# Performance work log

Hardware: AMD Instinct MI355X
Metric: run time of the kernel (lower is better)

The kernel has to match this reference:

```python
import jax, jax.numpy as jnp
import numpy as np

TRIM = 0.2
EPS = 1e-06
BIG = 1e30  # sentinel pushing invalid pixels to the end of the sort


def setup_inputs() -> dict:
    key = jax.random.key(0)
    k1, k2, k3 = jax.random.split(key, 3)
    B, C, H, W = 32, 1, 384, 1280
    pred = jax.random.normal(k1, (B, C, H, W), dtype=jnp.float32)
    gt = jax.random.normal(k2, (B, C, H, W), dtype=jnp.float32)
    mask = jax.random.randint(k3, (B, C, H, W), 0, 2, dtype=jnp.int32)
    return {"pred": pred, "gt": gt, "mask": mask}


def _per_sample_loss(p, g, m):
    # p, g: [N] float; m: [N] bool
    mf = m.astype(p.dtype)
    n = mf.sum()                      # number of valid pixels (float)
    n_safe = jnp.maximum(n, 1.0)
    # masked least-squares scale/shift: alpha = cov(d,z)/var(d), beta = mean_z - alpha*mean_d
    mean_d = jnp.sum(p * mf) / n_safe
    mean_z = jnp.sum(g * mf) / n_safe
    var_d = jnp.sum(p * p * mf) / n_safe - mean_d * mean_d
    cov_dz = jnp.sum(p * g * mf) / n_safe - mean_d * mean_z
    alpha = cov_dz / (var_d + EPS)
    beta = mean_z - alpha * mean_d
    # residuals; invalid pixels pushed to the tail of the sort
    res = jnp.abs(alpha * p + beta - g)
    res = jnp.where(m, res, BIG)
    res_sorted = jnp.sort(res)
    # keep the k = floor((1-trim)*n) smallest residuals
    k = jnp.floor((1.0 - TRIM) * n).astype(jnp.int32)
    keep = jnp.arange(res.shape[0], dtype=jnp.int32) < k
    kept_sum = jnp.sum(jnp.where(keep, res_sorted, 0.0))
    mean_kept = kept_sum / jnp.maximum(k.astype(p.dtype), 1.0)
    return jnp.where(k > 0, mean_kept, 0.0)


def reference(pred, gt, mask):
    B = pred.shape[0]
    p = pred.reshape(B, -1)
    g = gt.reshape(B, -1)
    m = mask.reshape(B, -1) > 0
    per_b = jax.vmap(_per_sample_loss)(p, g, m)  # [B]
    return jnp.mean(per_b)
```

## Files before the change

### kernel.cpp

```cpp
#include <hip/hip_runtime.h>
#include <stdint.h>

#define NB 32
#define NPIX 491520
#define NT 256

#define K1CHUNKS 60
#define K1CHUNK 8192
#define K1HALF4 (K1CHUNK / 8)
#define K1GROUPS (K1CHUNK / 4)
#define K1WORDS (K1CHUNK / 64)

#define K2CHUNKS 32
#define K2CHUNK 15360
#define K2IT (K2CHUNK / 4 / NT)
#define K2WORDS (K2CHUNK / 64)

#define NBINS 4096

#define CNT1 (1ull << 40)
#define SLOWMASK ((1ull << 40) - 1ull)

typedef float  vf4 __attribute__((ext_vector_type(4)));
typedef int    vi4 __attribute__((ext_vector_type(4)));

struct Ws {
  double moments[NB][5];
  double losses[NB];
  unsigned long long hist64[NB][NBINS];
};

__device__ __forceinline__ double wave_sum_d(double v) {
#pragma unroll
  for (int o = 32; o > 0; o >>= 1) v += __shfl_down(v, o, 64);
  return v;
}

__device__ __forceinline__ double block_sum_d(double v, double* red4) {
  v = wave_sum_d(v);
  const int lane = threadIdx.x & 63, w = threadIdx.x >> 6;
  if (lane == 0) red4[w] = v;
  __syncthreads();
  return red4[0] + red4[1] + red4[2] + red4[3];
}

__device__ __forceinline__ int k_from_n(double n) {
  return (int)floorf(0.8f * (float)n);
}

__device__ __forceinline__ void coef_from_moments(const Ws* ws, int b, float* a_out, float* be_out) {
  const double n = ws->moments[b][0];
  const double ns = n > 1.0 ? n : 1.0;
  const double md = ws->moments[b][1] / ns;
  const double mz = ws->moments[b][2] / ns;
  const double var = ws->moments[b][3] / ns - md * md;
  const double cov = ws->moments[b][4] / ns - md * mz;
  const double a = cov / (var + 1e-6);
  *a_out = (float)a;
  *be_out = (float)(mz - a * md);
}

__device__ __forceinline__ double bin_sum(int bin, unsigned long long h) {
  const double cnt = (double)(h >> 40);
  const double slow = (double)(h & SLOWMASK);
  const int e = bin >> 4, t4 = bin & 15;
  if (e == 0)
    return ldexp(cnt * (double)(t4 << 19) + slow, -149);
  return ldexp(cnt * (1.0 + (double)t4 * 0.0625) + slow * (1.0 / 8388608.0), e - 127);
}

template <bool BM>
__global__ __launch_bounds__(NT, 8) void k_mom(
    const float* __restrict__ pred, const float* __restrict__ gt,
    const int* __restrict__ mask, Ws* __restrict__ ws,
    unsigned long long* __restrict__ bm) {
  const int b = blockIdx.y;
  const size_t base = (size_t)b * NPIX + (size_t)blockIdx.x * K1CHUNK;
  const vf4* p4 = (const vf4*)(pred + base);
  const vf4* g4 = (const vf4*)(gt + base);
  const vi4* m4 = (const vi4*)(mask + base);
  __shared__ unsigned char nib[K1GROUPS];
  __shared__ double red4[4];
  float n = 0.f, sp = 0.f, sg = 0.f, spp = 0.f, spg = 0.f;
  for (int i = threadIdx.x; i < K1HALF4; i += NT) {
    vf4 pa = __builtin_nontemporal_load(&p4[i]);
    vf4 pb = __builtin_nontemporal_load(&p4[i + K1HALF4]);
    vf4 ga = __builtin_nontemporal_load(&g4[i]);
    vf4 gb = __builtin_nontemporal_load(&g4[i + K1HALF4]);
    vi4 ma = __builtin_nontemporal_load(&m4[i]);
    vi4 mb = __builtin_nontemporal_load(&m4[i + K1HALF4]);
    const float pe[8] = {pa.x, pa.y, pa.z, pa.w, pb.x, pb.y, pb.z, pb.w};
    const float ge[8] = {ga.x, ga.y, ga.z, ga.w, gb.x, gb.y, gb.z, gb.w};
    const int   me[8] = {ma.x, ma.y, ma.z, ma.w, mb.x, mb.y, mb.z, mb.w};
#pragma unroll
    for (int j = 0; j < 8; j++) {
      const float mf = me[j] ? 1.f : 0.f;
      const float pm = pe[j] * mf;
      const float gm = ge[j] * mf;
      n += mf; sp += pm; sg += gm;
      spp = fmaf(pe[j], pm, spp);
      spg = fmaf(pe[j], gm, spg);
    }
    if (BM) {
      nib[i] = (unsigned char)((me[0] ? 1 : 0) | (me[1] ? 2 : 0) |
                               (me[2] ? 4 : 0) | (me[3] ? 8 : 0));
      nib[i + K1HALF4] = (unsigned char)((me[4] ? 1 : 0) | (me[5] ? 2 : 0) |
                                         (me[6] ? 4 : 0) | (me[7] ? 8 : 0));
    }
  }
  if (BM) {
    __syncthreads();
    if (threadIdx.x < K1WORDS) {
      unsigned long long w = 0;
#pragma unroll
      for (int j = 0; j < 16; j++)
        w |= (unsigned long long)nib[threadIdx.x * 16 + j] << (4 * j);
      bm[base / 64 + threadIdx.x] = w;
    }
    __syncthreads();
  }
  double v[5] = {(double)n, (double)sp, (double)sg, (double)spp, (double)spg};
#pragma unroll
  for (int q = 0; q < 5; q++) {
    const double s = block_sum_d(v[q], red4);
    if (threadIdx.x == 0) atomicAdd(&ws->moments[b][q], s);
    __syncthreads();
  }
  const int flat = (b * K1CHUNKS + (int)blockIdx.x) * NT + (int)threadIdx.x;
  if (flat < NB * NBINS) ((unsigned long long*)ws->hist64)[flat] = 0ull;
}

template <bool BM>
__global__ __launch_bounds__(NT, 4) void k_hist(
    const float* __restrict__ pred, const float* __restrict__ gt,
    const int* __restrict__ mask, const unsigned long long* __restrict__ bm,
    Ws* __restrict__ ws) {
  __shared__ unsigned long long h64[NBINS];
  __shared__ unsigned long long smask[K2WORDS];
  for (int i = threadIdx.x; i < NBINS; i += NT) h64[i] = 0ull;
  const int b = blockIdx.y;
  const size_t base = (size_t)b * NPIX + (size_t)blockIdx.x * K2CHUNK;
  if (BM) {
    if (threadIdx.x < K2WORDS) smask[threadIdx.x] = bm[base / 64 + threadIdx.x];
  }
  float a, be;
  coef_from_moments(ws, b, &a, &be);
  __syncthreads();
  const vf4* p4 = (const vf4*)(pred + base);
  const vf4* g4 = (const vf4*)(gt + base);
  const vi4* m4 = (const vi4*)(mask + base);
  for (int j = 0; j < K2IT; j++) {
    const int i = j * NT + (int)threadIdx.x;
    const vf4 p = __builtin_nontemporal_load(&p4[i]);
    const vf4 g = __builtin_nontemporal_load(&g4[i]);
    const float pe[4] = {p.x, p.y, p.z, p.w};
    const float ge[4] = {g.x, g.y, g.z, g.w};
    int me[4];
    if (BM) {
      const unsigned int nb4 =
          (unsigned int)(smask[i >> 4] >> ((i & 15) * 4)) & 0xFu;
      me[0] = nb4 & 1; me[1] = nb4 & 2; me[2] = nb4 & 4; me[3] = nb4 & 8;
    } else {
      const vi4 m = __builtin_nontemporal_load(&m4[i]);
      me[0] = m.x; me[1] = m.y; me[2] = m.z; me[3] = m.w;
    }
#pragma unroll
    for (int l = 0; l < 4; l++) {
      if (!me[l]) continue;
      const float r = fabsf(fmaf(a, pe[l], be) - ge[l]);
      const uint32_t t = __float_as_uint(r);
      atomicAdd(&h64[t >> 19], CNT1 | (unsigned long long)(t & 0x7FFFFu));
    }
  }
  __syncthreads();
  for (int i = threadIdx.x; i < NBINS; i += NT) {
    const unsigned long long v = h64[i];
    if (v) atomicAdd(&ws->hist64[b][i], v);
  }
}

__global__ __launch_bounds__(NT) void k_fin(Ws* __restrict__ ws) {
  const int b = (int)blockIdx.x;
  const int tid = (int)threadIdx.x;
  __shared__ int pc[NT];
  __shared__ int shX, shCum;
  __shared__ double red4[4];
  const unsigned long long* H = ws->hist64[b];
  unsigned long long h[16];
  int lc = 0;
#pragma unroll
  for (int j = 0; j < 16; j++) { h[j] = H[tid * 16 + j]; lc += (int)(h[j] >> 40); }
  pc[tid] = lc;
  if (tid == 0) { shX = NBINS; shCum = 0; }
  __syncthreads();
  int pre = 0;
  for (int t = 0; t < tid; t++) pre += pc[t];
  const int k = k_from_n(ws->moments[b][0]);
  if (k > 0 && pre < k && pre + lc >= k) {
    int cum = pre;
#pragma unroll
    for (int j = 0; j < 16; j++) {
      const int c = (int)(h[j] >> 40);
      if (cum + c >= k) { shX = tid * 16 + j; shCum = cum; break; }
      cum += c;
    }
  }
  __syncthreads();
  const int X = shX;
  double below = 0.0;
#pragma unroll
  for (int j = 0; j < 16; j++) {
    const int idx = tid * 16 + j;
    if (idx < X) below += bin_sum(idx, h[j]);
  }
  const double tot = block_sum_d(below, red4);
  if (tid == 0) {
    double loss = 0.0;
    if (k > 0 && X < NBINS) {
      const unsigned long long hX = H[X];
      const double cX = (double)(hX >> 40);
      const double partial = (double)(k - shCum) * (bin_sum(X, hX) / cX);
      loss = (tot + partial) / (double)k;
    }
    ws->losses[b] = loss;
  }
}

__global__ void k_out(const Ws* __restrict__ ws, float* __restrict__ out) {
  double v = (threadIdx.x < NB) ? ws->losses[threadIdx.x] : 0.0;
  v = wave_sum_d(v);
  if (threadIdx.x == 0) out[0] = (float)(v / (double)NB);
}

extern "C" void kernel_launch(void* const* d_in, const int* in_sizes, int n_in,
                              void* d_out, int out_size, void* d_ws, size_t ws_size,
                              hipStream_t stream) {
  const float* pred = (const float*)d_in[0];
  const float* gt   = (const float*)d_in[1];
  const int*   mask = (const int*)d_in[2];
  float* out = (float*)d_out;
  Ws* ws = (Ws*)d_ws;

  const size_t boff = (sizeof(Ws) + 255) & ~(size_t)255;
  const size_t bbytes = (size_t)NB * NPIX / 8;
  const bool bm_ok = ws_size >= boff + bbytes;
  unsigned long long* bm = (unsigned long long*)((char*)d_ws + boff);

  (void)hipMemsetAsync(d_ws, 0, sizeof(double) * NB * 6, stream);

  dim3 g1(K1CHUNKS, NB);
  dim3 g2(K2CHUNKS, NB);
  if (bm_ok) {
    k_mom<true><<<g1, NT, 0, stream>>>(pred, gt, mask, ws, bm);
    k_hist<true><<<g2, NT, 0, stream>>>(pred, gt, mask, bm, ws);
  } else {
    k_mom<false><<<g1, NT, 0, stream>>>(pred, gt, mask, ws, nullptr);
    k_hist<false><<<g2, NT, 0, stream>>>(pred, gt, mask, nullptr, ws);
  }
  k_fin<<<NB, NT, 0, stream>>>(ws);
  k_out<<<1, 64, 0, stream>>>(ws, out);
}
```

Measured before the change: 209.6 us.

## Halve chunk sizes, use cached loads in moments pass, fold final reduction into k_fin

Grid chunk sizes for the moments and histogram kernels are halved, doubling the block count for better occupancy and load balance. The moments kernel unrolls its loop and drops nontemporal hints on pred/gt so the second pass can hit those lines in cache. The separate output kernel is removed: k_fin atomically accumulates per-sample losses and the last block writes the mean, saving one launch. Finer chunks double the atomics on moments and histograms, and the last-block pattern adds a fence and a counter that the memset must clear.

```diff
diff --git a/kernel.cpp b/kernel.cpp
--- a/kernel.cpp
+++ b/kernel.cpp
@@ -5,14 +5,14 @@
 #define NPIX 491520
 #define NT 256
 
-#define K1CHUNKS 60
-#define K1CHUNK 8192
+#define K1CHUNKS 120
+#define K1CHUNK 4096
 #define K1HALF4 (K1CHUNK / 8)
 #define K1GROUPS (K1CHUNK / 4)
 #define K1WORDS (K1CHUNK / 64)
 
-#define K2CHUNKS 32
-#define K2CHUNK 15360
+#define K2CHUNKS 60
+#define K2CHUNK 8192
 #define K2IT (K2CHUNK / 4 / NT)
 #define K2WORDS (K2CHUNK / 64)
 
@@ -26,7 +26,8 @@
 
 struct Ws {
   double moments[NB][5];
-  double losses[NB];
+  double loss_sum;
+  unsigned long long done;
   unsigned long long hist64[NB][NBINS];
 };
 
@@ -82,11 +83,14 @@
   __shared__ unsigned char nib[K1GROUPS];
   __shared__ double red4[4];
   float n = 0.f, sp = 0.f, sg = 0.f, spp = 0.f, spg = 0.f;
-  for (int i = threadIdx.x; i < K1HALF4; i += NT) {
-    vf4 pa = __builtin_nontemporal_load(&p4[i]);
-    vf4 pb = __builtin_nontemporal_load(&p4[i + K1HALF4]);
-    vf4 ga = __builtin_nontemporal_load(&g4[i]);
-    vf4 gb = __builtin_nontemporal_load(&g4[i + K1HALF4]);
+  const int t = (int)threadIdx.x;
+#pragma unroll
+  for (int u = 0; u < 2; u++) {
+    const int i = t + u * NT;
+    vf4 pa = p4[i];
+    vf4 pb = p4[i + K1HALF4];
+    vf4 ga = g4[i];
+    vf4 gb = g4[i + K1HALF4];
     vi4 ma = __builtin_nontemporal_load(&m4[i]);
     vi4 mb = __builtin_nontemporal_load(&m4[i + K1HALF4]);
     const float pe[8] = {pa.x, pa.y, pa.z, pa.w, pb.x, pb.y, pb.z, pb.w};
@@ -110,12 +114,12 @@
   }
   if (BM) {
     __syncthreads();
-    if (threadIdx.x < K1WORDS) {
+    if (t < K1WORDS) {
       unsigned long long w = 0;
 #pragma unroll
       for (int j = 0; j < 16; j++)
-        w |= (unsigned long long)nib[threadIdx.x * 16 + j] << (4 * j);
-      bm[base / 64 + threadIdx.x] = w;
+        w |= (unsigned long long)nib[t * 16 + j] << (4 * j);
+      bm[base / 64 + t] = w;
     }
     __syncthreads();
   }
@@ -123,10 +127,10 @@
 #pragma unroll
   for (int q = 0; q < 5; q++) {
     const double s = block_sum_d(v[q], red4);
-    if (threadIdx.x == 0) atomicAdd(&ws->moments[b][q], s);
+    if (t == 0) atomicAdd(&ws->moments[b][q], s);
     __syncthreads();
   }
-  const int flat = (b * K1CHUNKS + (int)blockIdx.x) * NT + (int)threadIdx.x;
+  const int flat = (b * K1CHUNKS + (int)blockIdx.x) * NT + t;
   if (flat < NB * NBINS) ((unsigned long long*)ws->hist64)[flat] = 0ull;
 }
 
@@ -149,6 +153,7 @@
   const vf4* p4 = (const vf4*)(pred + base);
   const vf4* g4 = (const vf4*)(gt + base);
   const vi4* m4 = (const vi4*)(mask + base);
+#pragma unroll 2
   for (int j = 0; j < K2IT; j++) {
     const int i = j * NT + (int)threadIdx.x;
     const vf4 p = __builtin_nontemporal_load(&p4[i]);
@@ -179,7 +184,7 @@
   }
 }
 
-__global__ __launch_bounds__(NT) void k_fin(Ws* __restrict__ ws) {
+__global__ __launch_bounds__(NT) void k_fin(Ws* __restrict__ ws, float* __restrict__ out) {
   const int b = (int)blockIdx.x;
   const int tid = (int)threadIdx.x;
   __shared__ int pc[NT];
@@ -222,14 +227,15 @@
       const double partial = (double)(k - shCum) * (bin_sum(X, hX) / cX);
       loss = (tot + partial) / (double)k;
     }
-    ws->losses[b] = loss;
-  }
-}
-
-__global__ void k_out(const Ws* __restrict__ ws, float* __restrict__ out) {
-  double v = (threadIdx.x < NB) ? ws->losses[threadIdx.x] : 0.0;
-  v = wave_sum_d(v);
-  if (threadIdx.x == 0) out[0] = (float)(v / (double)NB);
+    atomicAdd(&ws->loss_sum, loss);
+    __threadfence();
+    const unsigned long long old = atomicAdd(&ws->done, 1ull);
+    if (old == (unsigned long long)(NB - 1)) {
+      __threadfence();
+      const double sum = atomicAdd(&ws->loss_sum, 0.0);
+      out[0] = (float)(sum / (double)NB);
+    }
+  }
 }
 
 extern "C" void kernel_launch(void* const* d_in, const int* in_sizes, int n_in,
@@ -246,7 +252,7 @@
   const bool bm_ok = ws_size >= boff + bbytes;
   unsigned long long* bm = (unsigned long long*)((char*)d_ws + boff);
 
-  (void)hipMemsetAsync(d_ws, 0, sizeof(double) * NB * 6, stream);
+  (void)hipMemsetAsync(d_ws, 0, sizeof(double) * NB * 5 + 16, stream);
 
   dim3 g1(K1CHUNKS, NB);
   dim3 g2(K2CHUNKS, NB);
@@ -257,6 +263,5 @@
     k_mom<false><<<g1, NT, 0, stream>>>(pred, gt, mask, ws, nullptr);
     k_hist<false><<<g2, NT, 0, stream>>>(pred, gt, mask, nullptr, ws);
   }
-  k_fin<<<NB, NT, 0, stream>>>(ws);
-  k_out<<<1, 64, 0, stream>>>(ws, out);
-}
+  k_fin<<<NB, NT, 0, stream>>>(ws, out);
+}
```

Result: slower. 234.2 us (+11.7%).
